# Kernel tuning notes

Hardware: AMD Instinct MI355X
Metric: run time of the kernel (lower is better)

The kernel has to match this reference:

```python
import jax, jax.numpy as jnp
import numpy as np

N_NODES = 50000
E = 1600000
F_IN = 32
F_OUT = 32
N_CLASSES = 16


def setup_inputs() -> dict:
    key = jax.random.key(0)
    ks = jax.random.split(key, 20)
    s_in = 1.0 / np.sqrt(F_IN)
    s_cat = 1.0 / np.sqrt(2 * F_OUT)
    s_out = 1.0 / np.sqrt(F_OUT)
    inp = {
        "x": jax.random.normal(ks[0], (N_NODES, F_IN), dtype=jnp.float32),
        "edge_index": jax.random.randint(ks[1], (2, E), 0, N_NODES, dtype=jnp.int64),
        "edge_weight": jax.random.uniform(ks[2], (E,), dtype=jnp.float32),
        # GCNConv weights for z, r, h gates: [F_IN, F_OUT] + bias [F_OUT]
        "Wz": jax.random.uniform(ks[3], (F_IN, F_OUT), minval=-s_in, maxval=s_in),
        "bz": jnp.zeros((F_OUT,), jnp.float32),
        "Wr": jax.random.uniform(ks[4], (F_IN, F_OUT), minval=-s_in, maxval=s_in),
        "br": jnp.zeros((F_OUT,), jnp.float32),
        "Wh": jax.random.uniform(ks[5], (F_IN, F_OUT), minval=-s_in, maxval=s_in),
        "bh": jnp.zeros((F_OUT,), jnp.float32),
        # Gate linears: Linear(2*F_OUT, F_OUT) stored as [2*F_OUT, F_OUT]
        "Lz_w": jax.random.uniform(ks[6], (2 * F_OUT, F_OUT), minval=-s_cat, maxval=s_cat),
        "Lz_b": jax.random.uniform(ks[7], (F_OUT,), minval=-s_cat, maxval=s_cat),
        "Lr_w": jax.random.uniform(ks[8], (2 * F_OUT, F_OUT), minval=-s_cat, maxval=s_cat),
        "Lr_b": jax.random.uniform(ks[9], (F_OUT,), minval=-s_cat, maxval=s_cat),
        "Lh_w": jax.random.uniform(ks[10], (2 * F_OUT, F_OUT), minval=-s_cat, maxval=s_cat),
        "Lh_b": jax.random.uniform(ks[11], (F_OUT,), minval=-s_cat, maxval=s_cat),
        # Output linear: Linear(F_OUT, N_CLASSES) stored as [F_OUT, N_CLASSES]
        "W_out": jax.random.uniform(ks[12], (F_OUT, N_CLASSES), minval=-s_out, maxval=s_out),
        "b_out": jax.random.uniform(ks[13], (N_CLASSES,), minval=-s_out, maxval=s_out),
    }
    return inp


def reference(x, edge_index, edge_weight, Wz, bz, Wr, br, Wh, bh,
              Lz_w, Lz_b, Lr_w, Lr_b, Lh_w, Lh_b, W_out, b_out):
    N = x.shape[0]
    src, dst = edge_index[0], edge_index[1]
    loops = jnp.arange(N)
    # GCNConv default: add self-loops (weight 1) + symmetric normalization
    src_f = jnp.concatenate([src, loops])
    dst_f = jnp.concatenate([dst, loops])
    ew_f = jnp.concatenate([edge_weight, jnp.ones((N,), x.dtype)])
    deg = jax.ops.segment_sum(ew_f, dst_f, num_segments=N)
    dinv = jnp.where(deg > 0, jax.lax.rsqrt(jnp.where(deg > 0, deg, 1.0)), 0.0)
    norm = dinv[src_f] * ew_f * dinv[dst_f]  # [E+N]

    def gcn(W, b):
        xw = x @ W  # [N, F_OUT]
        return jax.ops.segment_sum(norm[:, None] * xw[src_f], dst_f, num_segments=N) + b

    H = jnp.zeros((N, Wz.shape[1]), x.dtype)  # initial hidden state
    Z = jax.nn.sigmoid(jnp.concatenate([gcn(Wz, bz), H], axis=1) @ Lz_w + Lz_b)
    R = jax.nn.sigmoid(jnp.concatenate([gcn(Wr, br), H], axis=1) @ Lr_w + Lr_b)
    H_tilde = jnp.tanh(jnp.concatenate([gcn(Wh, bh), H * R], axis=1) @ Lh_w + Lh_b)
    H = Z * H + (1.0 - Z) * H_tilde

    h = jax.nn.relu(H)
    logits = h @ W_out + b_out
    return jax.nn.softmax(logits, axis=1)
```

## Files before the change

kernel.cpp:

```cpp
#include <hip/hip_runtime.h>

#define NN 50000
#define NE 1600000
#define NPB 32
#define NBIN ((NN + NPB - 1) / NPB)
#define NBH 128
#define CHE (NE / NBH)
#define HALF 25000
#define WBLK 256
#define EPB (NE / WBLK)
#define CAP 2048


__global__ __launch_bounds__(1024) void k_deghist(const int* __restrict__ ei,
                                                  const float* __restrict__ ew,
                                                  float* __restrict__ deg,
                                                  unsigned* __restrict__ gbincnt) {
    __shared__ float hist[HALF];
    __shared__ unsigned bcnt[NBIN];
    int p = blockIdx.x >> 7;
    int c = blockIdx.x & 127;
    int base = p * HALF;
    for (int i = threadIdx.x; i < HALF; i += 1024) hist[i] = 0.f;
    if (p == 0)
        for (int i = threadIdx.x; i < NBIN; i += 1024) bcnt[i] = 0u;
    __syncthreads();
    int lo = c * CHE, hi = lo + CHE;
    for (int e = lo + threadIdx.x; e < hi; e += 1024) {
        int d = ei[NE + e];
        if (p == 0) atomicAdd(&bcnt[d >> 5], 1u);
        unsigned r = (unsigned)(d - base);
        if (r < HALF) atomicAdd(&hist[r], ew[e]);
    }
    __syncthreads();
    for (int i = threadIdx.x; i < HALF; i += 1024)
        atomicAdd(&deg[base + i], hist[i]);
    if (p == 0)
        for (int i = threadIdx.x; i < NBIN; i += 1024)
            if (bcnt[i]) atomicAdd(&gbincnt[i], bcnt[i]);
}

__global__ __launch_bounds__(256) void k_mid(
        const float* __restrict__ deg, float* __restrict__ dinv,
        const unsigned* __restrict__ gbincnt, unsigned* __restrict__ binstart,
        unsigned* __restrict__ bincur,
        const float* __restrict__ Wz, const float* __restrict__ Lzw,
        const float* __restrict__ bz, const float* __restrict__ Lzb,
        const float* __restrict__ Wh, const float* __restrict__ Lhw,
        const float* __restrict__ bh, const float* __restrict__ Lhb,
        float* __restrict__ Mz, float* __restrict__ Mh,
        float* __restrict__ cz, float* __restrict__ chv) {
    int t = threadIdx.x, b = blockIdx.x;
    if (b == 0) {
        __shared__ unsigned ts[256];
        unsigned v[7], s = 0;
#pragma unroll
        for (int r = 0; r < 7; ++r) {
            int idx = t * 7 + r;
            v[r] = (idx < NBIN) ? gbincnt[idx] : 0u;
            s += v[r];
        }
        ts[t] = s;
        __syncthreads();
        for (int off = 1; off < 256; off <<= 1) {
            unsigned u = (t >= off) ? ts[t - off] : 0u;
            __syncthreads();
            ts[t] += u;
            __syncthreads();
        }
        unsigned acc = (t > 0) ? ts[t - 1] : 0u;
#pragma unroll
        for (int r = 0; r < 7; ++r) {
            int idx = t * 7 + r;
            if (idx < NBIN) { binstart[idx] = acc; bincur[idx] = acc; }
            acc += v[r];
        }
        if (t == 0) binstart[NBIN] = NE;
    } else if (b == 1) {
#pragma unroll
        for (int r = 0; r < 4; ++r) {
            int t2 = r * 256 + t;
            int i = t2 >> 5, j = t2 & 31;
            float sz = 0.f, sh = 0.f;
            for (int k = 0; k < 32; ++k) {
                sz += Wz[i * 32 + k] * Lzw[k * 32 + j];
                sh += Wh[i * 32 + k] * Lhw[k * 32 + j];
            }
            Mz[t2] = sz;
            Mh[t2] = sh;
        }
        if (t < 32) {
            float az = Lzb[t], ah = Lhb[t];
            for (int k = 0; k < 32; ++k) {
                az += bz[k] * Lzw[k * 32 + t];
                ah += bh[k] * Lhw[k * 32 + t];
            }
            cz[t] = az;
            chv[t] = ah;
        }
    } else {
        int n = (b - 2) * 256 + t;
        if (n < NN) dinv[n] = rsqrtf(deg[n] + 1.0f);
    }
}

__global__ __launch_bounds__(512) void k_binwrite(const int* __restrict__ ei,
                                                  const float* __restrict__ ew,
                                                  const float* __restrict__ dinv,
                                                  unsigned* __restrict__ bincur,
                                                  float2* __restrict__ er) {
    __shared__ unsigned cnt[NBIN], base[NBIN];
    int t = threadIdx.x;
    for (int i = t; i < NBIN; i += 512) cnt[i] = 0u;
    __syncthreads();
    int lo = blockIdx.x * EPB, hi = lo + EPB;
    for (int e = lo + t; e < hi; e += 512)
        atomicAdd(&cnt[ei[NE + e] >> 5], 1u);
    __syncthreads();
    for (int i = t; i < NBIN; i += 512)
        base[i] = cnt[i] ? atomicAdd(&bincur[i], cnt[i]) : 0u;
    __syncthreads();
    for (int e = lo + t; e < hi; e += 512) {
        int s = ei[e], d = ei[NE + e];
        float v = dinv[s] * ew[e];
        unsigned idx = atomicAdd(&base[d >> 5], 1u);
        er[idx] = make_float2(
            __uint_as_float((unsigned)s | ((unsigned)(d & 31) << 16)), v);
    }
}

__global__ __launch_bounds__(256) void k_accum(
        const float2* __restrict__ er, const unsigned* __restrict__ binstart,
        const float* __restrict__ dinv, const float* __restrict__ x,
        float* __restrict__ Aout) {
    __shared__ float2 srt[CAP];
    __shared__ unsigned cnt4[4][32];
    __shared__ unsigned base4[4][32];
    __shared__ unsigned rowp[33];
    const float4* x4 = (const float4*)x;
    int t = threadIdx.x;
    int w = t >> 6;
    unsigned beg = binstart[blockIdx.x], end = binstart[blockIdx.x + 1];
    unsigned cntb = end - beg;
    unsigned stage = cntb < CAP ? cntb : CAP;

    if (t < 128) ((unsigned*)cnt4)[t] = 0u;
    __syncthreads();

    float2 rec[8];
    unsigned dlk[8];
    bool val[8];
#pragma unroll
    for (int k = 0; k < 8; ++k) {
        unsigned i = (unsigned)t + (unsigned)k * 256u;
        val[k] = (i < stage);
        if (val[k]) {
            float2 r = er[beg + i];
            rec[k] = r;
            unsigned d = (__float_as_uint(r.x) >> 16) & 31u;
            dlk[k] = d;
            atomicAdd(&cnt4[w][d], 1u);
        }
    }
    __syncthreads();

    if (t < 32) {
        unsigned s = 0;
#pragma unroll
        for (int ww = 0; ww < 4; ++ww) {
            unsigned c = cnt4[ww][t];
            base4[ww][t] = s;
            s += c;
        }
        unsigned tot = s;
#pragma unroll
        for (int off = 1; off < 32; off <<= 1) {
            unsigned v = __shfl_up(tot, off, 32);
            if (t >= off) tot += v;
        }
        unsigned excl = tot - s;
        rowp[t] = excl;
        if (t == 31) rowp[32] = excl + s;
#pragma unroll
        for (int ww = 0; ww < 4; ++ww) base4[ww][t] += excl;
    }
    __syncthreads();

#pragma unroll
    for (int k = 0; k < 8; ++k) {
        if (val[k]) {
            unsigned p = atomicAdd(&base4[w][dlk[k]], 1u);
            srt[p] = rec[k];
        }
    }
    __syncthreads();

    int l = t >> 3, j = t & 7;
    int n = blockIdx.x * NPB + l;
    float4 acc = make_float4(0.f, 0.f, 0.f, 0.f);
    unsigned rb = rowp[l], re = rowp[l + 1];
    unsigned i = rb;
    for (; i + 4 <= re; i += 4) {
        float2 r0 = srt[i], r1 = srt[i + 1], r2 = srt[i + 2], r3 = srt[i + 3];
        unsigned s0 = __float_as_uint(r0.x) & 0xFFFFu;
        unsigned s1 = __float_as_uint(r1.x) & 0xFFFFu;
        unsigned s2 = __float_as_uint(r2.x) & 0xFFFFu;
        unsigned s3 = __float_as_uint(r3.x) & 0xFFFFu;
        float4 a0 = x4[s0 * 8 + j];
        float4 a1 = x4[s1 * 8 + j];
        float4 a2 = x4[s2 * 8 + j];
        float4 a3 = x4[s3 * 8 + j];
        acc.x += r0.y * a0.x; acc.y += r0.y * a0.y; acc.z += r0.y * a0.z; acc.w += r0.y * a0.w;
        acc.x += r1.y * a1.x; acc.y += r1.y * a1.y; acc.z += r1.y * a1.z; acc.w += r1.y * a1.w;
        acc.x += r2.y * a2.x; acc.y += r2.y * a2.y; acc.z += r2.y * a2.z; acc.w += r2.y * a2.w;
        acc.x += r3.y * a3.x; acc.y += r3.y * a3.y; acc.z += r3.y * a3.z; acc.w += r3.y * a3.w;
    }
    for (; i < re; ++i) {
        float2 r = srt[i];
        unsigned s = __float_as_uint(r.x) & 0xFFFFu;
        float4 a = x4[s * 8 + j];
        acc.x += r.y * a.x; acc.y += r.y * a.y; acc.z += r.y * a.z; acc.w += r.y * a.w;
    }
    for (unsigned o = stage; o < cntb; ++o) {
        float2 r = er[beg + o];
        unsigned pk = __float_as_uint(r.x);
        if (((pk >> 16) & 31u) == (unsigned)l) {
            float4 a = x4[(pk & 0xFFFFu) * 8 + j];
            acc.x += r.y * a.x; acc.y += r.y * a.y; acc.z += r.y * a.z; acc.w += r.y * a.w;
        }
    }
    if (n < NN) {
        float dv = dinv[n];
        float4 xv = x4[n * 8 + j];
        float4 o;
        o.x = dv * (acc.x + dv * xv.x);
        o.y = dv * (acc.y + dv * xv.y);
        o.z = dv * (acc.z + dv * xv.z);
        o.w = dv * (acc.w + dv * xv.w);
        ((float4*)Aout)[n * 8 + j] = o;
    }
}

__global__ __launch_bounds__(256) void k_dense(
        const float* __restrict__ Aout, const float* __restrict__ Mz,
        const float* __restrict__ Mh, const float* __restrict__ cz,
        const float* __restrict__ chv, const float* __restrict__ Wout,
        const float* __restrict__ bout, float* __restrict__ out) {
    __shared__ float sMz[1024], sMh[1024], sW[512], scz[32], sch[32], sb[16];
    __shared__ float sA[8][32];
    int tid = threadIdx.x;
    for (int i = tid; i < 1024; i += 256) { sMz[i] = Mz[i]; sMh[i] = Mh[i]; }
    for (int i = tid; i < 512; i += 256) sW[i] = Wout[i];
    if (tid < 32) { scz[tid] = cz[tid]; sch[tid] = chv[tid]; }
    if (tid < 16) sb[tid] = bout[tid];

    int g = tid >> 5, f = tid & 31;
    int n = blockIdx.x * 8 + g;
    float av = Aout[(size_t)n * 32 + f];
    sA[g][f] = av;
    __syncthreads();

    float z = scz[f], gh = sch[f];
#pragma unroll
    for (int k = 0; k < 32; ++k) {
        float ak = sA[g][k];
        z += ak * sMz[k * 32 + f];
        gh += ak * sMh[k * 32 + f];
    }
    z = 1.0f / (1.0f + expf(-z));
    gh = tanhf(gh);
    float hv = (1.0f - z) * gh;
    hv = hv > 0.f ? hv : 0.f;
    __syncthreads();
    sA[g][f] = hv;
    __syncthreads();

    if (f < 16) {
        float lg = sb[f];
#pragma unroll
        for (int j = 0; j < 32; ++j) lg += sA[g][j] * sW[j * 16 + f];
        float mx = lg;
#pragma unroll
        for (int w = 8; w >= 1; w >>= 1) mx = fmaxf(mx, __shfl_xor(mx, w, 16));
        float p = expf(lg - mx);
        float sum = p;
#pragma unroll
        for (int w = 8; w >= 1; w >>= 1) sum += __shfl_xor(sum, w, 16);
        out[n * 16 + f] = p / sum;
    }
}

extern "C" void kernel_launch(void* const* d_in, const int* in_sizes, int n_in,
                              void* d_out, int out_size, void* d_ws, size_t ws_size,
                              hipStream_t stream) {
    const float* x    = (const float*)d_in[0];
    const int*   ei   = (const int*)d_in[1];
    const float* ew   = (const float*)d_in[2];
    const float* Wz   = (const float*)d_in[3];
    const float* bz   = (const float*)d_in[4];
    const float* Wh   = (const float*)d_in[7];
    const float* bh   = (const float*)d_in[8];
    const float* Lzw  = (const float*)d_in[9];
    const float* Lzb  = (const float*)d_in[10];
    const float* Lhw  = (const float*)d_in[13];
    const float* Lhb  = (const float*)d_in[14];
    const float* Wout = (const float*)d_in[15];
    const float* bout = (const float*)d_in[16];
    float* out = (float*)d_out;

    float* ws = (float*)d_ws;
    float2*   er       = (float2*)ws;
    float*    Aout     = ws + 2 * (size_t)NE;
    float*    deg      = Aout + (size_t)NN * 32;
    unsigned* gbincnt  = (unsigned*)(deg + NN);
    float*    dinv     = (float*)(gbincnt + NBIN);
    unsigned* binstart = (unsigned*)(dinv + NN);
    unsigned* bincur   = binstart + NBIN + 1;
    float*    Mz       = (float*)(bincur + NBIN);
    float*    Mh       = Mz + 1024;
    float*    cz       = Mh + 1024;
    float*    chv      = cz + 32;

    hipMemsetAsync(deg, 0, (NN + NBIN) * sizeof(float), stream);

    k_deghist<<<2 * NBH, 1024, 0, stream>>>(ei, ew, deg, gbincnt);
    k_mid<<<2 + (NN + 255) / 256, 256, 0, stream>>>(deg, dinv, gbincnt, binstart,
                                                    bincur, Wz, Lzw, bz, Lzb,
                                                    Wh, Lhw, bh, Lhb, Mz, Mh, cz, chv);
    k_binwrite<<<WBLK, 512, 0, stream>>>(ei, ew, dinv, bincur, er);
    k_accum<<<NBIN, 256, 0, stream>>>(er, binstart, dinv, x, Aout);
    k_dense<<<NN / 8, 256, 0, stream>>>(Aout, Mz, Mh, cz, chv, Wout, bout, out);
}
```

Baseline: 151.7 us.

## Derive degrees from binned edges and split bin counters per XCD

Replaces the large shared-memory degree histogram kernel with a light bin-count kernel. Degrees are now computed per bin from the already-bucketed edge records in a new k_deg kernel, and the source-side dinv scaling moves into k_accum. Global bin counters and cursors are replicated eight ways, indexed by block id modulo 8 (per XCD), to reduce cross-die atomic contention. The cost is an extra pass over the edge records and an extra launch, in exchange for dropping the 25000-entry float histogram and its global atomics.

```diff
diff --git a/kernel.cpp b/kernel.cpp
--- a/kernel.cpp
+++ b/kernel.cpp
@@ -4,61 +4,45 @@
 #define NE 1600000
 #define NPB 32
 #define NBIN ((NN + NPB - 1) / NPB)
-#define NBH 128
-#define CHE (NE / NBH)
-#define HALF 25000
-#define WBLK 256
+#define NXCD 8
+#define WBLK 512
 #define EPB (NE / WBLK)
 #define CAP 2048
 
 
-__global__ __launch_bounds__(1024) void k_deghist(const int* __restrict__ ei,
-                                                  const float* __restrict__ ew,
-                                                  float* __restrict__ deg,
-                                                  unsigned* __restrict__ gbincnt) {
-    __shared__ float hist[HALF];
-    __shared__ unsigned bcnt[NBIN];
-    int p = blockIdx.x >> 7;
-    int c = blockIdx.x & 127;
-    int base = p * HALF;
-    for (int i = threadIdx.x; i < HALF; i += 1024) hist[i] = 0.f;
-    if (p == 0)
-        for (int i = threadIdx.x; i < NBIN; i += 1024) bcnt[i] = 0u;
-    __syncthreads();
-    int lo = c * CHE, hi = lo + CHE;
-    for (int e = lo + threadIdx.x; e < hi; e += 1024) {
-        int d = ei[NE + e];
-        if (p == 0) atomicAdd(&bcnt[d >> 5], 1u);
-        unsigned r = (unsigned)(d - base);
-        if (r < HALF) atomicAdd(&hist[r], ew[e]);
-    }
-    __syncthreads();
-    for (int i = threadIdx.x; i < HALF; i += 1024)
-        atomicAdd(&deg[base + i], hist[i]);
-    if (p == 0)
-        for (int i = threadIdx.x; i < NBIN; i += 1024)
-            if (bcnt[i]) atomicAdd(&gbincnt[i], bcnt[i]);
+__global__ __launch_bounds__(256) void k_cnt(const int* __restrict__ ei,
+                                             unsigned* __restrict__ gbincnt8) {
+    __shared__ unsigned cnt[NBIN];
+    int t = threadIdx.x;
+    int xcd = blockIdx.x & (NXCD - 1);
+    for (int i = t; i < NBIN; i += 256) cnt[i] = 0u;
+    __syncthreads();
+    int lo = blockIdx.x * EPB, hi = lo + EPB;
+    for (int e = lo + t; e < hi; e += 256)
+        atomicAdd(&cnt[ei[NE + e] >> 5], 1u);
+    __syncthreads();
+    for (int i = t; i < NBIN; i += 256)
+        if (cnt[i]) atomicAdd(&gbincnt8[xcd * NBIN + i], cnt[i]);
 }
 
 __global__ __launch_bounds__(256) void k_mid(
-        const float* __restrict__ deg, float* __restrict__ dinv,
-        const unsigned* __restrict__ gbincnt, unsigned* __restrict__ binstart,
-        unsigned* __restrict__ bincur,
+        const unsigned* __restrict__ gbincnt8, unsigned* __restrict__ binstart,
+        unsigned* __restrict__ bincur8,
         const float* __restrict__ Wz, const float* __restrict__ Lzw,
         const float* __restrict__ bz, const float* __restrict__ Lzb,
         const float* __restrict__ Wh, const float* __restrict__ Lhw,
         const float* __restrict__ bh, const float* __restrict__ Lhb,
         float* __restrict__ Mz, float* __restrict__ Mh,
         float* __restrict__ cz, float* __restrict__ chv) {
-    int t = threadIdx.x, b = blockIdx.x;
-    if (b == 0) {
+    int t = threadIdx.x;
+    if (blockIdx.x == 0) {
         __shared__ unsigned ts[256];
-        unsigned v[7], s = 0;
+        unsigned s = 0;
 #pragma unroll
         for (int r = 0; r < 7; ++r) {
             int idx = t * 7 + r;
-            v[r] = (idx < NBIN) ? gbincnt[idx] : 0u;
-            s += v[r];
+            if (idx < NBIN)
+                for (int x = 0; x < NXCD; ++x) s += gbincnt8[x * NBIN + idx];
         }
         ts[t] = s;
         __syncthreads();
@@ -72,11 +56,16 @@
 #pragma unroll
         for (int r = 0; r < 7; ++r) {
             int idx = t * 7 + r;
-            if (idx < NBIN) { binstart[idx] = acc; bincur[idx] = acc; }
-            acc += v[r];
-        }
-        if (t == 0) binstart[NBIN] = NE;
-    } else if (b == 1) {
+            if (idx < NBIN) {
+                binstart[idx] = acc;
+                for (int x = 0; x < NXCD; ++x) {
+                    bincur8[x * NBIN + idx] = acc;
+                    acc += gbincnt8[x * NBIN + idx];
+                }
+            }
+        }
+        if (t == 255) binstart[NBIN] = NE;
+    } else {
 #pragma unroll
         for (int r = 0; r < 4; ++r) {
             int t2 = r * 256 + t;
@@ -98,34 +87,49 @@
             cz[t] = az;
             chv[t] = ah;
         }
-    } else {
-        int n = (b - 2) * 256 + t;
-        if (n < NN) dinv[n] = rsqrtf(deg[n] + 1.0f);
-    }
-}
-
-__global__ __launch_bounds__(512) void k_binwrite(const int* __restrict__ ei,
+    }
+}
+
+__global__ __launch_bounds__(256) void k_binwrite(const int* __restrict__ ei,
                                                   const float* __restrict__ ew,
-                                                  const float* __restrict__ dinv,
-                                                  unsigned* __restrict__ bincur,
+                                                  unsigned* __restrict__ bincur8,
                                                   float2* __restrict__ er) {
     __shared__ unsigned cnt[NBIN], base[NBIN];
     int t = threadIdx.x;
-    for (int i = t; i < NBIN; i += 512) cnt[i] = 0u;
+    int xcd = blockIdx.x & (NXCD - 1);
+    for (int i = t; i < NBIN; i += 256) cnt[i] = 0u;
     __syncthreads();
     int lo = blockIdx.x * EPB, hi = lo + EPB;
-    for (int e = lo + t; e < hi; e += 512)
+    for (int e = lo + t; e < hi; e += 256)
         atomicAdd(&cnt[ei[NE + e] >> 5], 1u);
     __syncthreads();
-    for (int i = t; i < NBIN; i += 512)
-        base[i] = cnt[i] ? atomicAdd(&bincur[i], cnt[i]) : 0u;
-    __syncthreads();
-    for (int e = lo + t; e < hi; e += 512) {
+    for (int i = t; i < NBIN; i += 256)
+        base[i] = cnt[i] ? atomicAdd(&bincur8[xcd * NBIN + i], cnt[i]) : 0u;
+    __syncthreads();
+    for (int e = lo + t; e < hi; e += 256) {
         int s = ei[e], d = ei[NE + e];
-        float v = dinv[s] * ew[e];
         unsigned idx = atomicAdd(&base[d >> 5], 1u);
         er[idx] = make_float2(
-            __uint_as_float((unsigned)s | ((unsigned)(d & 31) << 16)), v);
+            __uint_as_float((unsigned)s | ((unsigned)(d & 31) << 16)), ew[e]);
+    }
+}
+
+__global__ __launch_bounds__(256) void k_deg(const float2* __restrict__ er,
+                                             const unsigned* __restrict__ binstart,
+                                             float* __restrict__ dinv) {
+    __shared__ float degL[NPB];
+    int t = threadIdx.x;
+    if (t < NPB) degL[t] = 0.f;
+    __syncthreads();
+    unsigned beg = binstart[blockIdx.x], end = binstart[blockIdx.x + 1];
+    for (unsigned i = beg + t; i < end; i += 256) {
+        float2 r = er[i];
+        atomicAdd(&degL[(__float_as_uint(r.x) >> 16) & 31u], r.y);
+    }
+    __syncthreads();
+    if (t < NPB) {
+        int n = blockIdx.x * NPB + t;
+        if (n < NN) dinv[n] = rsqrtf(degL[t] + 1.0f);
     }
 }
 
@@ -156,8 +160,10 @@
         val[k] = (i < stage);
         if (val[k]) {
             float2 r = er[beg + i];
+            unsigned pk = __float_as_uint(r.x);
+            r.y *= dinv[pk & 0xFFFFu];
             rec[k] = r;
-            unsigned d = (__float_as_uint(r.x) >> 16) & 31u;
+            unsigned d = (pk >> 16) & 31u;
             dlk[k] = d;
             atomicAdd(&cnt4[w][d], 1u);
         }
@@ -225,8 +231,10 @@
         float2 r = er[beg + o];
         unsigned pk = __float_as_uint(r.x);
         if (((pk >> 16) & 31u) == (unsigned)l) {
-            float4 a = x4[(pk & 0xFFFFu) * 8 + j];
-            acc.x += r.y * a.x; acc.y += r.y * a.y; acc.z += r.y * a.z; acc.w += r.y * a.w;
+            unsigned s = pk & 0xFFFFu;
+            float4 a = x4[s * 8 + j];
+            float v = r.y * dinv[s];
+            acc.x += v * a.x; acc.y += v * a.y; acc.z += v * a.z; acc.w += v * a.w;
         }
     }
     if (n < NN) {
@@ -311,23 +319,23 @@
     float* ws = (float*)d_ws;
     float2*   er       = (float2*)ws;
     float*    Aout     = ws + 2 * (size_t)NE;
-    float*    deg      = Aout + (size_t)NN * 32;
-    unsigned* gbincnt  = (unsigned*)(deg + NN);
-    float*    dinv     = (float*)(gbincnt + NBIN);
-    unsigned* binstart = (unsigned*)(dinv + NN);
-    unsigned* bincur   = binstart + NBIN + 1;
-    float*    Mz       = (float*)(bincur + NBIN);
+    float*    dinv     = Aout + (size_t)NN * 32;
+    unsigned* gbincnt8 = (unsigned*)(dinv + NN);
+    unsigned* binstart = gbincnt8 + NXCD * NBIN;
+    unsigned* bincur8  = binstart + NBIN + 1;
+    float*    Mz       = (float*)(bincur8 + NXCD * NBIN);
     float*    Mh       = Mz + 1024;
     float*    cz       = Mh + 1024;
     float*    chv      = cz + 32;
 
-    hipMemsetAsync(deg, 0, (NN + NBIN) * sizeof(float), stream);
-
-    k_deghist<<<2 * NBH, 1024, 0, stream>>>(ei, ew, deg, gbincnt);
-    k_mid<<<2 + (NN + 255) / 256, 256, 0, stream>>>(deg, dinv, gbincnt, binstart,
-                                                    bincur, Wz, Lzw, bz, Lzb,
-                                                    Wh, Lhw, bh, Lhb, Mz, Mh, cz, chv);
-    k_binwrite<<<WBLK, 512, 0, stream>>>(ei, ew, dinv, bincur, er);
+    hipMemsetAsync(gbincnt8, 0, NXCD * NBIN * sizeof(unsigned), stream);
+
+    k_cnt<<<WBLK, 256, 0, stream>>>(ei, gbincnt8);
+    k_mid<<<2, 256, 0, stream>>>(gbincnt8, binstart, bincur8,
+                                 Wz, Lzw, bz, Lzb, Wh, Lhw, bh, Lhb,
+                                 Mz, Mh, cz, chv);
+    k_binwrite<<<WBLK, 256, 0, stream>>>(ei, ew, bincur8, er);
+    k_deg<<<NBIN, 256, 0, stream>>>(er, binstart, dinv);
     k_accum<<<NBIN, 256, 0, stream>>>(er, binstart, dinv, x, Aout);
     k_dense<<<NN / 8, 256, 0, stream>>>(Aout, Mz, Mh, cz, chv, Wout, bout, out);
 }
```

Result: faster. 123.6 us (-18.6%).
